# Performance work log

Hardware: AMD Instinct MI355X
Metric: run time of the kernel (lower is better)

Reference implementation:

```python
import jax, jax.numpy as jnp
import numpy as np

N = 50000        # nodes
E = 400000       # edges per relation graph
IN_DIM = 64
HID = 128
OUT_DIM = 2
NSEL = 4096
EPS = 0.3        # residual scale
SLOPE = 0.3      # LeakyReLU negative slope


def _leaky(x):
    return jnp.where(x >= 0, x, SLOPE * x)


def _deg_norm(dst):
    # FAGCN-style d = in_degree^{-1/2}; 0 for isolated nodes
    deg = jax.ops.segment_sum(jnp.ones(dst.shape[0], jnp.float32), dst, num_segments=N)
    return jnp.where(deg > 0, jax.lax.rsqrt(jnp.maximum(deg, 1.0)), 0.0)


def _gnn_layer(hf, src, dst, d, gw, gb):
    # gate(concat[h_dst, h_src]) computed as per-node projections then edge gather
    D = hf.shape[1]
    s_dst = hf @ gw[:D]   # [N]
    s_src = hf @ gw[D:]   # [N]
    a = jnp.tanh(s_dst[dst] + s_src[src] + gb)        # [E]
    e = a * d[dst] * d[src]                            # [E]
    msg = hf[src] * e[:, None]                         # [E, D]
    return jax.ops.segment_sum(msg, dst, num_segments=N)


def setup_inputs() -> dict:
    key = jax.random.key(0)
    ks = iter(jax.random.split(key, 48))
    def nrm(shape, scale=0.05):
        return jax.random.normal(next(ks), shape, jnp.float32) * scale
    inp = {}
    inp["h"] = jax.random.normal(next(ks), (N, IN_DIM), jnp.float32)
    for i in (1, 2, 3):
        inp[f"src{i}"] = jax.random.randint(next(ks), (E,), 0, N)
        inp[f"dst{i}"] = jax.random.randint(next(ks), (E,), 0, N)
    inp["nodes"] = jax.random.randint(next(ks), (NSEL,), 0, N)
    inp["t1_w"] = nrm((HID, IN_DIM)); inp["t1_b"] = jnp.zeros((HID,), jnp.float32)
    for i in (1, 2, 3):
        inp[f"gate1_{i}_w"] = nrm((2 * HID,)); inp[f"gate1_{i}_b"] = jnp.zeros((), jnp.float32)
        inp[f"gate2_{i}_w"] = nrm((6 * HID,)); inp[f"gate2_{i}_b"] = jnp.zeros((), jnp.float32)
        inp[f"hw1_{i}"] = nrm((HID, HID))
        inp[f"hw2_{i}"] = nrm((3 * HID, HID))
    inp["t2_w"] = nrm((64, 7 * HID + IN_DIM)); inp["t2_b"] = jnp.zeros((64,), jnp.float32)
    inp["t3_w"] = nrm((OUT_DIM, 64)); inp["t3_b"] = jnp.zeros((OUT_DIM,), jnp.float32)
    return inp


def reference(h, src1, dst1, src2, dst2, src3, dst3, nodes,
              t1_w, t1_b,
              gate1_1_w, gate1_1_b, gate1_2_w, gate1_2_b, gate1_3_w, gate1_3_b,
              gate2_1_w, gate2_1_b, gate2_2_w, gate2_2_b, gate2_3_w, gate2_3_b,
              hw1_1, hw1_2, hw1_3, hw2_1, hw2_2, hw2_3,
              t2_w, t2_b, t3_w, t3_b):
    d1, d2, d3 = _deg_norm(dst1), _deg_norm(dst2), _deg_norm(dst3)
    raw0 = h
    raw1 = _leaky(h @ t1_w.T + t1_b)   # [N, HID] (dropout=identity in eval)
    h1_1 = _leaky((EPS * raw1 + _gnn_layer(raw1, src1, dst1, d1, gate1_1_w, gate1_1_b)) @ hw1_1)
    h1_2 = _leaky((EPS * raw1 + _gnn_layer(raw1, src2, dst2, d2, gate1_2_w, gate1_2_b)) @ hw1_2)
    h1_3 = _leaky((EPS * raw1 + _gnn_layer(raw1, src3, dst3, d3, gate1_3_w, gate1_3_b)) @ hw1_3)
    raw2 = jnp.concatenate([h1_1, h1_2, h1_3], axis=1)   # [N, 3*HID]
    h2_1 = _leaky((EPS * raw2 + _gnn_layer(raw2, src1, dst1, d1, gate2_1_w, gate2_1_b)) @ hw2_1)
    h2_2 = _leaky((EPS * raw2 + _gnn_layer(raw2, src2, dst2, d2, gate2_2_w, gate2_2_b)) @ hw2_2)
    h2_3 = _leaky((EPS * raw2 + _gnn_layer(raw2, src3, dst3, d3, gate2_3_w, gate2_3_b)) @ hw2_3)
    hf = jnp.concatenate([h2_1, h2_2, h2_3, raw0, raw1, raw2], axis=1)  # [N, 7*HID+IN_DIM]
    nf = hf[nodes]                                       # [NSEL, 7*HID+IN_DIM]
    s = _leaky(nf @ t2_w.T + t2_b)
    return s @ t3_w.T + t3_b                             # [NSEL, OUT_DIM]
```

## Files before the change

### kernel.cpp

```cpp
#include <hip/hip_runtime.h>
#include <hip/hip_bf16.h>

#define NN 50000
#define NE 400000
#define IND 64
#define HID 128
#define H3 384
#define FDIM 960
#define NSEL 4096
#define EPSF 0.3f
#define SLOPEF 0.3f
#define NBK 196
#define BCAP 4096
#define EPB 4096
#define NOEDGE 0xFFFFFFFFu
#define NBF 98

typedef __attribute__((ext_vector_type(8))) short bfrag;
typedef __attribute__((ext_vector_type(4))) float f4;
typedef __attribute__((ext_vector_type(8))) unsigned short us8;

__device__ __forceinline__ float leaky1(float v){ return v>=0.f? v : SLOPEF*v; }
__device__ __forceinline__ float b2f(unsigned short u){
  return __uint_as_float(((unsigned)u)<<16);
}
__device__ __forceinline__ unsigned short f2b(float v){
  __hip_bfloat16 b = __float2bfloat16(v);
  return *(unsigned short*)&b;
}

__global__ __launch_bounds__(256) void k_fill_prep(
    const int* __restrict__ s0,const int* __restrict__ d0,
    const int* __restrict__ s1,const int* __restrict__ d1,
    const int* __restrict__ s2,const int* __restrict__ d2,
    int* __restrict__ bcnt, unsigned int* __restrict__ pairbuf,
    const float* __restrict__ t1w,
    const float* __restrict__ hw1_0, const float* __restrict__ hw1_1, const float* __restrict__ hw1_2,
    const float* __restrict__ hw2_0, const float* __restrict__ hw2_1, const float* __restrict__ hw2_2,
    const float* __restrict__ t2w, const float* __restrict__ h,
    unsigned short* __restrict__ wt1, unsigned short* __restrict__ w1t,
    unsigned short* __restrict__ w2t, unsigned short* __restrict__ wt2,
    unsigned short* __restrict__ hb)
{
  __shared__ __align__(16) unsigned int lbuf[EPB];
  __shared__ int hist[256];
  __shared__ int lbase[256];
  __shared__ int lcur[256];
  __shared__ int gbase[NBK];
  __shared__ int wsum[4];
  const int t = threadIdx.x;

  if (blockIdx.x < 3*NBF){
    const int r = blockIdx.x / NBF;
    const int bx = blockIdx.x - r*NBF;
    const int* S = (r==0)?s0:((r==1)?s1:s2);
    const int* D = (r==0)?d0:((r==1)?d1:d2);
    const int e0 = bx*EPB;
    hist[t] = 0; lcur[t] = 0;
    __syncthreads();
    unsigned int pv[16];
    #pragma unroll
    for (int j=0;j<4;j++){
      int e = e0 + (j*256 + t)*4;
      if (e < NE){
        int4 sv = *(const int4*)&S[e];
        int4 dv = *(const int4*)&D[e];
        pv[j*4+0] = ((unsigned)dv.x<<16)|(unsigned)sv.x;
        pv[j*4+1] = ((unsigned)dv.y<<16)|(unsigned)sv.y;
        pv[j*4+2] = ((unsigned)dv.z<<16)|(unsigned)sv.z;
        pv[j*4+3] = ((unsigned)dv.w<<16)|(unsigned)sv.w;
      } else {
        pv[j*4+0]=NOEDGE; pv[j*4+1]=NOEDGE; pv[j*4+2]=NOEDGE; pv[j*4+3]=NOEDGE;
      }
    }
    #pragma unroll
    for (int i=0;i<16;i++){
      if (pv[i] != NOEDGE) atomicAdd(&hist[pv[i]>>24], 1);
    }
    __syncthreads();
    {
      int hv = hist[t];
      int lane = t & 63, wid = t >> 6;
      int x = hv;
      #pragma unroll
      for (int d=1; d<64; d<<=1){ int y=__shfl_up(x,(unsigned)d); if(lane>=d) x+=y; }
      if (lane==63) wsum[wid]=x;
      __syncthreads();
      int wpre = 0;
      if (wid>0) wpre += wsum[0];
      if (wid>1) wpre += wsum[1];
      if (wid>2) wpre += wsum[2];
      lbase[t] = wpre + x - hv;
      if (t < NBK){
        int hh = hist[t];
        gbase[t] = (hh>0) ? atomicAdd(&bcnt[r*NBK+t], hh) : 0;
      }
    }
    __syncthreads();
    #pragma unroll
    for (int i=0;i<16;i++){
      if (pv[i] != NOEDGE){
        int b = (int)(pv[i] >> 24);
        int pos = lbase[b] + atomicAdd(&lcur[b], 1);
        lbuf[pos] = pv[i];
      }
    }
    __syncthreads();
    int tot = min(NE - e0, EPB);
    for (int idx = t; idx < tot; idx += 256){
      unsigned int v = lbuf[idx];
      int b = (int)(v >> 24);
      pairbuf[((size_t)(r*NBK + b))*BCAP + gbase[b] + (idx - lbase[b])] = v;
    }
  } else {
    int g = (blockIdx.x - 3*NBF)*256 + t;
    if (g < 8192){
      wt1[g] = f2b(t1w[g]);
    } else if (g < 57344){
      int e = g - 8192;
      int r = e / 16384, q = e - r*16384;
      int n = q >> 7, k = q & 127;
      const float* W = (r==0)?hw1_0:((r==1)?hw1_1:hw1_2);
      w1t[e] = f2b(W[k*HID + n]);
    } else if (g < 204800){
      int e = g - 57344;
      int r = e / 49152, q = e - r*49152;
      int n = q / H3, k = q - n*H3;
      const float* W = (r==0)?hw2_0:((r==1)?hw2_1:hw2_2);
      w2t[e] = f2b(W[k*HID + n]);
    } else if (g < 266240){
      int e = g - 204800;
      wt2[e] = f2b(t2w[e]);
    } else if (g < 666240){
      int q = g - 266240;
      const float4 a = ((const float4*)h)[q*2];
      const float4 b = ((const float4*)h)[q*2+1];
      us8 o;
      o[0]=f2b(a.x); o[1]=f2b(a.y); o[2]=f2b(a.z); o[3]=f2b(a.w);
      o[4]=f2b(b.x); o[5]=f2b(b.y); o[6]=f2b(b.z); o[7]=f2b(b.w);
      *(us8*)&hb[q*8] = o;
    }
  }
}

__global__ __launch_bounds__(256) void k_sort_t1(
    const unsigned int* __restrict__ pairbuf, const int* __restrict__ bcnt,
    int* __restrict__ off, float* __restrict__ dnv, unsigned short* __restrict__ csrc,
    const unsigned short* __restrict__ Ab, const unsigned short* __restrict__ W,
    const float* __restrict__ bias, unsigned short* __restrict__ Cb)
{
  __shared__ __align__(16) char smem[27648];
  const int t = threadIdx.x;

  if (blockIdx.x < 2*NBK + NBK){
    unsigned short* lout = (unsigned short*)smem;
    int* hist = (int*)(smem + 8192);
    int* excl = (int*)(smem + 9216);
    int* cur  = (int*)(smem + 10240);
    int* red  = (int*)(smem + 11264);
    int* wsum = (int*)(smem + 12288);
    const int r = blockIdx.x / NBK;
    const int b = blockIdx.x - r*NBK;
    const int nb0 = b << 8;
    red[t] = (t < b) ? bcnt[r*NBK + t] : 0;
    hist[t] = 0; cur[t] = 0;
    __syncthreads();
    #pragma unroll
    for (int sdv=128; sdv>0; sdv>>=1){
      if (t < sdv) red[t] += red[t+sdv];
      __syncthreads();
    }
    const int bbase = red[0];
    const int cnt = bcnt[r*NBK + b];
    const unsigned int* pb = pairbuf + ((size_t)(r*NBK + b))*BCAP;
    unsigned int pv[16];
    #pragma unroll
    for (int j=0;j<16;j++){
      int e = j*256 + t;
      pv[j] = (e < cnt) ? pb[e] : NOEDGE;
      if (pv[j] != NOEDGE) atomicAdd(&hist[(int)(pv[j]>>16) - nb0], 1);
    }
    __syncthreads();
    {
      int hv = hist[t];
      int lane = t & 63, wid = t >> 6;
      int x = hv;
      #pragma unroll
      for (int d=1; d<64; d<<=1){ int y=__shfl_up(x,(unsigned)d); if(lane>=d) x+=y; }
      if (lane==63) wsum[wid]=x;
      __syncthreads();
      int wpre = 0;
      if (wid>0) wpre += wsum[0];
      if (wid>1) wpre += wsum[1];
      if (wid>2) wpre += wsum[2];
      excl[t] = wpre + x - hv;
    }
    __syncthreads();
    int nidx = nb0 + t;
    if (nidx < NN){
      off[r*(NN+1) + nidx] = bbase + excl[t];
      int g = hist[t];
      dnv[r*NN + nidx] = (g>0) ? rsqrtf((float)g) : 0.f;
    }
    if (b == NBK-1 && t == 0) off[r*(NN+1) + NN] = bbase + cnt;
    #pragma unroll
    for (int j=0;j<16;j++){
      if (pv[j] != NOEDGE){
        int pn = (int)(pv[j] >> 16) - nb0;
        int slot = atomicAdd(&cur[pn], 1);
        lout[excl[pn] + slot] = (unsigned short)(pv[j] & 0xffffu);
      }
    }
    __syncthreads();
    unsigned short* op = csrc + (size_t)r*NE + bbase;
    for (int idx = t; idx < cnt; idx += 256) op[idx] = lout[idx];
  } else {
    short (*As)[72] = (short(*)[72])smem;
    short (*Bs)[72] = (short(*)[72])(smem + 9216);
    const int bm = (blockIdx.x - 3*NBK)*64;
    for (int q = t; q < 64*8; q += 256){
      int row = q >> 3, c8 = q & 7;
      int grow = bm + row; grow = (grow < NN) ? grow : (NN-1);
      *(us8*)&As[row][c8*8] = *(const us8*)&Ab[(size_t)grow*IND + c8*8];
    }
    for (int q = t; q < 128*8; q += 256){
      int n = q >> 3, c8 = q & 7;
      *(us8*)&Bs[n][c8*8] = *(const us8*)&W[n*IND + c8*8];
    }
    __syncthreads();
    const int wid = t >> 6, lane = t & 63;
    const int wrow = (wid & 1)*32, wcol = (wid >> 1)*64;
    const int fr = lane & 15, fq = lane >> 4;
    f4 acc[2][4];
    #pragma unroll
    for (int mi=0;mi<2;mi++)
      #pragma unroll
      for (int ni=0;ni<4;ni++) acc[mi][ni] = (f4){0.f,0.f,0.f,0.f};
    #pragma unroll
    for (int ks=0; ks<2; ks++){
      int kb = ks*32 + fq*8;
      bfrag a[2], b[4];
      #pragma unroll
      for (int mi=0;mi<2;mi++) a[mi] = *(const bfrag*)&As[wrow + mi*16 + fr][kb];
      #pragma unroll
      for (int ni=0;ni<4;ni++) b[ni] = *(const bfrag*)&Bs[wcol + ni*16 + fr][kb];
      #pragma unroll
      for (int mi=0;mi<2;mi++)
        #pragma unroll
        for (int ni=0;ni<4;ni++)
          acc[mi][ni] = __builtin_amdgcn_mfma_f32_16x16x32_bf16(a[mi], b[ni], acc[mi][ni], 0, 0, 0);
    }
    #pragma unroll
    for (int mi=0;mi<2;mi++){
      int row0 = bm + wrow + mi*16 + fq*4;
      #pragma unroll
      for (int j=0;j<4;j++){
        int row = row0 + j;
        if (row < NN){
          #pragma unroll
          for (int ni=0;ni<4;ni++){
            int col = wcol + ni*16 + fr;
            Cb[(size_t)row*HID + col] = f2b(leaky1(acc[mi][ni][j] + bias[col]));
          }
        }
      }
    }
  }
}

__global__ __launch_bounds__(256) void k_mfma128(
    const unsigned short* __restrict__ Abf, const unsigned short* __restrict__ Wt,
    unsigned short* __restrict__ Cb, int M)
{
  __shared__ short As[64][136];
  __shared__ short Bs[128][136];
  const int r = blockIdx.y;
  const unsigned short* Ar = Abf + (size_t)r*M*HID;
  const unsigned short* W  = Wt + (size_t)r*HID*HID;
  const int tid = threadIdx.x;
  const int bm = blockIdx.x*64;

  for (int q = tid; q < 64*16; q += 256){
    int row = q >> 4, c8 = q & 15;
    int grow = bm + row; grow = (grow < M) ? grow : (M-1);
    *(us8*)&As[row][c8*8] = *(const us8*)&Ar[(size_t)grow*HID + c8*8];
  }
  for (int q = tid; q < 128*16; q += 256){
    int n = q >> 4, c8 = q & 15;
    *(us8*)&Bs[n][c8*8] = *(const us8*)&W[n*HID + c8*8];
  }
  __syncthreads();

  const int wid = tid >> 6, lane = tid & 63;
  const int wrow = (wid & 1)*32, wcol = (wid >> 1)*64;
  const int fr = lane & 15, fq = lane >> 4;
  f4 acc[2][4];
  #pragma unroll
  for (int mi=0;mi<2;mi++)
    #pragma unroll
    for (int ni=0;ni<4;ni++) acc[mi][ni] = (f4){0.f,0.f,0.f,0.f};

  #pragma unroll
  for (int ks=0; ks<4; ks++){
    int kb = ks*32 + fq*8;
    bfrag a[2], b[4];
    #pragma unroll
    for (int mi=0;mi<2;mi++) a[mi] = *(const bfrag*)&As[wrow + mi*16 + fr][kb];
    #pragma unroll
    for (int ni=0;ni<4;ni++) b[ni] = *(const bfrag*)&Bs[wcol + ni*16 + fr][kb];
    #pragma unroll
    for (int mi=0;mi<2;mi++)
      #pragma unroll
      for (int ni=0;ni<4;ni++)
        acc[mi][ni] = __builtin_amdgcn_mfma_f32_16x16x32_bf16(a[mi], b[ni], acc[mi][ni], 0, 0, 0);
  }

  const int coff = r*HID;
  #pragma unroll
  for (int mi=0;mi<2;mi++){
    int row0 = bm + wrow + mi*16 + fq*4;
    #pragma unroll
    for (int j=0;j<4;j++){
      int row = row0 + j;
      if (row < M){
        #pragma unroll
        for (int ni=0;ni<4;ni++){
          Cb[(size_t)row*H3 + coff + wcol + ni*16 + fr] = f2b(leaky1(acc[mi][ni][j]));
        }
      }
    }
  }
}

__global__ __launch_bounds__(256) void k_hw2_nf(
    const unsigned short* __restrict__ Abf, const unsigned short* __restrict__ Wt,
    const unsigned short* __restrict__ hb, const unsigned short* __restrict__ raw1b,
    const unsigned short* __restrict__ raw2b, const int* __restrict__ nodes,
    unsigned short* __restrict__ nfb)
{
  __shared__ __align__(16) char smem[23040];
  const int t = threadIdx.x;
  if (blockIdx.x < 3*128){
    short (*As)[72] = (short(*)[72])smem;
    short (*Bs)[72] = (short(*)[72])(smem + 4608);
    const int r = blockIdx.x / 128;
    const int bm = (blockIdx.x - r*128)*32;
    const unsigned short* Ar = Abf + (size_t)r*NSEL*H3;
    const unsigned short* W  = Wt + (size_t)r*HID*H3;
    const int wid = t >> 6, lane = t & 63;
    const int fr = lane & 15, fq = lane >> 4;
    f4 acc[2][2];
    #pragma unroll
    for (int mi=0;mi<2;mi++)
      #pragma unroll
      for (int ni=0;ni<2;ni++) acc[mi][ni] = (f4){0.f,0.f,0.f,0.f};
    for (int kc=0; kc<6; kc++){
      for (int q = t; q < 32*8; q += 256){
        int row = q >> 3, c8 = q & 7;
        *(us8*)&As[row][c8*8] = *(const us8*)&Ar[(size_t)(bm+row)*H3 + kc*64 + c8*8];
      }
      for (int q = t; q < 128*8; q += 256){
        int n = q >> 3, c8 = q & 7;
        *(us8*)&Bs[n][c8*8] = *(const us8*)&W[(size_t)n*H3 + kc*64 + c8*8];
      }
      __syncthreads();
      #pragma unroll
      for (int ks=0; ks<2; ks++){
        int kb = ks*32 + fq*8;
        bfrag a[2], b[2];
        #pragma unroll
        for (int mi=0;mi<2;mi++) a[mi] = *(const bfrag*)&As[mi*16 + fr][kb];
        #pragma unroll
        for (int ni=0;ni<2;ni++) b[ni] = *(const bfrag*)&Bs[wid*32 + ni*16 + fr][kb];
        #pragma unroll
        for (int mi=0;mi<2;mi++)
          #pragma unroll
          for (int ni=0;ni<2;ni++)
            acc[mi][ni] = __builtin_amdgcn_mfma_f32_16x16x32_bf16(a[mi], b[ni], acc[mi][ni], 0, 0, 0);
      }
      __syncthreads();
    }
    #pragma unroll
    for (int mi=0;mi<2;mi++){
      int row0 = bm + mi*16 + fq*4;
      #pragma unroll
      for (int j=0;j<4;j++){
        int i = row0 + j;
        #pragma unroll
        for (int ni=0;ni<2;ni++){
          int col = wid*32 + ni*16 + fr;
          nfb[(size_t)i*FDIM + r*HID + col] = f2b(leaky1(acc[mi][ni][j]));
        }
      }
    }
  } else {
    int g = (blockIdx.x - 3*128)*256 + t;
    if (g < NSEL*72){
      int i = g/72, c = g - i*72;
      int n = nodes[i];
      us8 v; int col;
      if (c < 8)       { v = *(const us8*)&hb[(size_t)n*IND + c*8];           col = 384 + c*8; }
      else if (c < 24) { int q=c-8;  v = *(const us8*)&raw1b[(size_t)n*HID + q*8]; col = 448 + q*8; }
      else             { int q=c-24; v = *(const us8*)&raw2b[(size_t)n*H3  + q*8]; col = 576 + q*8; }
      *(us8*)&nfb[(size_t)i*FDIM + col] = v;
    }
  }
}

__global__ __launch_bounds__(256) void k_t2_final(
    const unsigned short* __restrict__ Abf, const unsigned short* __restrict__ W,
    const float* __restrict__ t2b, const float* __restrict__ t3w,
    const float* __restrict__ t3b, float* __restrict__ outp)
{
  __shared__ __align__(16) char smem[13824];
  short (*As)[72] = (short(*)[72])smem;
  short (*Bs)[72] = (short(*)[72])(smem + 4608);
  float (*sb)[64] = (float(*)[64])smem;
  const int t = threadIdx.x;
  const int bm = blockIdx.x*32;
  const int wid = t >> 6, lane = t & 63;
  const int fr = lane & 15, fq = lane >> 4;
  f4 acc[2];
  acc[0] = (f4){0.f,0.f,0.f,0.f};
  acc[1] = (f4){0.f,0.f,0.f,0.f};

  for (int kc=0; kc<15; kc++){
    for (int q = t; q < 32*8; q += 256){
      int row = q >> 3, c8 = q & 7;
      *(us8*)&As[row][c8*8] = *(const us8*)&Abf[(size_t)(bm+row)*FDIM + kc*64 + c8*8];
    }
    for (int q = t; q < 64*8; q += 256){
      int n = q >> 3, c8 = q & 7;
      *(us8*)&Bs[n][c8*8] = *(const us8*)&W[(size_t)n*FDIM + kc*64 + c8*8];
    }
    __syncthreads();
    #pragma unroll
    for (int ks=0; ks<2; ks++){
      int kb = ks*32 + fq*8;
      bfrag a[2], b;
      a[0] = *(const bfrag*)&As[fr][kb];
      a[1] = *(const bfrag*)&As[16 + fr][kb];
      b = *(const bfrag*)&Bs[wid*16 + fr][kb];
      acc[0] = __builtin_amdgcn_mfma_f32_16x16x32_bf16(a[0], b, acc[0], 0, 0, 0);
      acc[1] = __builtin_amdgcn_mfma_f32_16x16x32_bf16(a[1], b, acc[1], 0, 0, 0);
    }
    __syncthreads();
  }

  #pragma unroll
  for (int mi=0;mi<2;mi++){
    int rloc = mi*16 + fq*4;
    #pragma unroll
    for (int j=0;j<4;j++){
      sb[rloc+j][wid*16 + fr] = acc[mi][j];
    }
  }
  __syncthreads();
  for (int rr = wid*8; rr < wid*8+8; rr++){
    float v = leaky1(sb[rr][lane] + t2b[lane]);
    float a0 = v*t3w[lane], a1 = v*t3w[64+lane];
    #pragma unroll
    for (int sft=32;sft>0;sft>>=1){
      a0 += __shfl_down(a0,(unsigned)sft);
      a1 += __shfl_down(a1,(unsigned)sft);
    }
    if (lane==0){
      int w = bm + rr;
      outp[2*w+0] = a0 + t3b[0];
      outp[2*w+1] = a1 + t3b[1];
    }
  }
}

template<int D>
__global__ __launch_bounds__(256) void k_scores_g(const unsigned short* __restrict__ X,
    const float* __restrict__ g0, const float* __restrict__ g1, const float* __restrict__ g2,
    float* __restrict__ sd, float* __restrict__ ss){
  const int tid = threadIdx.x;
  const int p = tid & 15;
  const int n = blockIdx.x*16 + (tid >> 4);
  const unsigned short* x = X + (size_t)n*D;
  float a0=0,a1=0,a2=0,a3=0,a4=0,a5=0;
  #pragma unroll
  for (int it=0; it<D/128; it++){
    int k = it*128 + p*8;
    us8 u = *(const us8*)&x[k];
    #pragma unroll
    for (int e=0;e<8;e++){
      float v = b2f(u[e]);
      a0 = fmaf(v, g0[k+e],   a0);  a1 = fmaf(v, g0[D+k+e], a1);
      a2 = fmaf(v, g1[k+e],   a2);  a3 = fmaf(v, g1[D+k+e], a3);
      a4 = fmaf(v, g2[k+e],   a4);  a5 = fmaf(v, g2[D+k+e], a5);
    }
  }
  #pragma unroll
  for (int s=8;s>0;s>>=1){
    a0 += __shfl_xor(a0,(unsigned)s); a1 += __shfl_xor(a1,(unsigned)s);
    a2 += __shfl_xor(a2,(unsigned)s); a3 += __shfl_xor(a3,(unsigned)s);
    a4 += __shfl_xor(a4,(unsigned)s); a5 += __shfl_xor(a5,(unsigned)s);
  }
  if (p==0){
    sd[0*NN+n]=a0; ss[0*NN+n]=a1;
    sd[1*NN+n]=a2; ss[1*NN+n]=a3;
    sd[2*NN+n]=a4; ss[2*NN+n]=a5;
  }
}

__global__ __launch_bounds__(256) void k_gather_f3z(
    const unsigned short* __restrict__ Xb,
    const int* __restrict__ off, const unsigned short* __restrict__ csrc,
    const float* __restrict__ sd, const float* __restrict__ ss,
    const float* __restrict__ dnv,
    const float* __restrict__ gb0, const float* __restrict__ gb1, const float* __restrict__ gb2,
    unsigned short* __restrict__ outp){
  const int tid = threadIdx.x;
  const int lane = tid & 63;
  const int wg = lane >> 4;
  const int p  = lane & 15;
  const int n = blockIdx.x*16 + (tid >> 4);
  us8 rv = *(const us8*)&Xb[(size_t)n*HID + p*8];
  int p0a[3], p1a[3];
  #pragma unroll
  for (int r=0;r<3;r++){
    p0a[r] = off[r*(NN+1) + n];
    p1a[r] = off[r*(NN+1) + n + 1];
  }
  float resid[8];
  #pragma unroll
  for (int i=0;i<8;i++) resid[i] = EPSF * b2f(rv[i]);

  for (int r=0;r<3;r++){
    const unsigned short* csr = csrc + (size_t)r*NE;
    const float* ssr = ss + r*NN;
    const float* dnr = dnv + r*NN;
    float gbv = ((r==0)?gb0:((r==1)?gb1:gb2))[0];
    float sd_n = sd[r*NN + n], dn_n = dnr[n];
    float acc[8];
    #pragma unroll
    for (int i=0;i<8;i++) acc[i] = resid[i];
    int p0 = p0a[r], p1 = p1a[r];
    for (int pc=p0; pc<p1; pc+=16){
      int m = min(16, p1-pc);
      int s = 0; float c = 0.f;
      if (p < m){
        s = csr[pc+p];
        c = tanhf(sd_n + ssr[s] + gbv) * dn_n * dnr[s];
      }
      int   sj = __shfl(s, wg*16);
      float cj = __shfl(c, wg*16);
      us8 v = *(const us8*)&Xb[(size_t)sj*HID + p*8];
      for (int j=1;j<=m;j++){
        us8 vn; float cn = 0.f;
        if (j < m){
          int sn = __shfl(s, wg*16+j);
          cn = __shfl(c, wg*16+j);
          vn = *(const us8*)&Xb[(size_t)sn*HID + p*8];
        }
        #pragma unroll
        for (int i=0;i<8;i++) acc[i] = fmaf(cj, b2f(v[i]), acc[i]);
        v = vn; cj = cn;
      }
    }
    us8 o;
    #pragma unroll
    for (int i=0;i<8;i++) o[i] = f2b(acc[i]);
    *(us8*)&outp[((size_t)r*NN + n)*HID + p*8] = o;
  }
}

__global__ __launch_bounds__(256) void k_gather_sel3w2(const unsigned short* __restrict__ Xb,
    const int* __restrict__ nodes,
    const int* __restrict__ off, const unsigned short* __restrict__ csrc,
    const float* __restrict__ sd, const float* __restrict__ ss,
    const float* __restrict__ dnv,
    const float* __restrict__ gb0, const float* __restrict__ gb1, const float* __restrict__ gb2,
    unsigned short* __restrict__ outp){
  const int tid = threadIdx.x;
  const int lane = tid & 63;
  const int wg = lane >> 4;
  const int p  = lane & 15;
  const int i = blockIdx.x*16 + (tid >> 4);
  const int r = blockIdx.y;
  const int n = nodes[i];
  const int* offr = off + r*(NN+1);
  const unsigned short* csr = csrc + (size_t)r*NE;
  const float* ssr = ss + r*NN;
  const float* dnr = dnv + r*NN;
  float gbv = ((r==0)?gb0:((r==1)?gb1:gb2))[0];
  float sd_n = sd[r*NN + n], dn_n = dnr[n];
  float acc[3][8];
  #pragma unroll
  for (int cc=0;cc<3;cc++)
    #pragma unroll
    for (int q=0;q<8;q++) acc[cc][q]=0.f;
  int p0 = offr[n], p1 = offr[n+1];
  for (int pc=p0; pc<p1; pc+=16){
    int m = min(16, p1-pc);
    int s = 0; float c = 0.f;
    if (p < m){
      s = csr[pc+p];
      c = tanhf(sd_n + ssr[s] + gbv) * dn_n * dnr[s];
    }
    int   sj = __shfl(s, wg*16);
    float cj = __shfl(c, wg*16);
    const unsigned short* row = &Xb[(size_t)sj*H3];
    us8 v0 = *(const us8*)&row[0*HID + p*8];
    us8 v1 = *(const us8*)&row[1*HID + p*8];
    us8 v2 = *(const us8*)&row[2*HID + p*8];
    for (int j=1;j<=m;j++){
      us8 n0, n1, n2; float cn = 0.f;
      if (j < m){
        int sn = __shfl(s, wg*16+j);
        cn = __shfl(c, wg*16+j);
        const unsigned short* rw = &Xb[(size_t)sn*H3];
        n0 = *(const us8*)&rw[0*HID + p*8];
        n1 = *(const us8*)&rw[1*HID + p*8];
        n2 = *(const us8*)&rw[2*HID + p*8];
      }
      #pragma unroll
      for (int q=0;q<8;q++){
        acc[0][q] = fmaf(cj, b2f(v0[q]), acc[0][q]);
        acc[1][q] = fmaf(cj, b2f(v1[q]), acc[1][q]);
        acc[2][q] = fmaf(cj, b2f(v2[q]), acc[2][q]);
      }
      v0 = n0; v1 = n1; v2 = n2; cj = cn;
    }
  }
  const unsigned short* xrow = &Xb[(size_t)n*H3];
  unsigned short* orow = &outp[((size_t)r*NSEL + i)*H3];
  #pragma unroll
  for (int cc=0;cc<3;cc++){
    us8 v = *(const us8*)&xrow[cc*HID + p*8];
    us8 o;
    #pragma unroll
    for (int q=0;q<8;q++) o[q] = f2b(fmaf(EPSF, b2f(v[q]), acc[cc][q]));
    *(us8*)&orow[cc*HID + p*8] = o;
  }
}

extern "C" void kernel_launch(void* const* d_in, const int* in_sizes, int n_in,
                              void* d_out, int out_size, void* d_ws, size_t ws_size,
                              hipStream_t stream){
  if (n_in < 32) return;
  const float* h = (const float*)d_in[0];
  const int* src[3] = {(const int*)d_in[1], (const int*)d_in[3], (const int*)d_in[5]};
  const int* dst[3] = {(const int*)d_in[2], (const int*)d_in[4], (const int*)d_in[6]};
  const int* nodes = (const int*)d_in[7];
  const float* t1w = (const float*)d_in[8];
  const float* t1b = (const float*)d_in[9];

  bool dictOrder = (in_sizes[12] == 768);
  const float *g1w[3],*g1b[3],*g2w[3],*g2b[3],*hw1[3],*hw2[3];
  for (int r=0;r<3;r++){
    if (dictOrder){
      int base = 10 + r*6;
      g1w[r]=(const float*)d_in[base+0]; g1b[r]=(const float*)d_in[base+1];
      g2w[r]=(const float*)d_in[base+2]; g2b[r]=(const float*)d_in[base+3];
      hw1[r]=(const float*)d_in[base+4]; hw2[r]=(const float*)d_in[base+5];
    } else {
      g1w[r]=(const float*)d_in[10+2*r]; g1b[r]=(const float*)d_in[11+2*r];
      g2w[r]=(const float*)d_in[16+2*r]; g2b[r]=(const float*)d_in[17+2*r];
      hw1[r]=(const float*)d_in[22+r];   hw2[r]=(const float*)d_in[25+r];
    }
  }
  const float* t2w = (const float*)d_in[28];
  const float* t2b = (const float*)d_in[29];
  const float* t3w = (const float*)d_in[30];
  const float* t3b = (const float*)d_in[31];
  float* outp = (float*)d_out;

  char* w = (char*)d_ws;
  auto carve = [&](size_t bytes)->void*{
    void* p = (void*)w;
    w += ((bytes + 255) & ~size_t(255));
    return p;
  };
  int*   bcnt = (int*)  carve((size_t)1024*4);
  int*   off  = (int*)  carve((size_t)3*(NN+1)*4);
  float* dnv  = (float*)carve((size_t)3*NN*4);
  unsigned short* csrc = (unsigned short*)carve((size_t)3*NE*2);
  float* sd1  = (float*)carve((size_t)3*NN*4);
  float* ss1  = (float*)carve((size_t)3*NN*4);
  float* sd2  = (float*)carve((size_t)3*NN*4);
  float* ss2  = (float*)carve((size_t)3*NN*4);
  unsigned short* wt1 = (unsigned short*)carve((size_t)HID*IND*2);
  unsigned short* w1t = (unsigned short*)carve((size_t)3*HID*HID*2);
  unsigned short* w2t = (unsigned short*)carve((size_t)3*HID*H3*2);
  unsigned short* wt2 = (unsigned short*)carve((size_t)64*FDIM*2);
  unsigned short* hb  = (unsigned short*)carve((size_t)NN*IND*2);
  unsigned short* raw1b = (unsigned short*)carve((size_t)NN*HID*2);
  unsigned short* raw2b = (unsigned short*)carve((size_t)NN*H3*2);
  size_t ubytes = (size_t)3*NN*HID*2;
  float* ureg = (float*)carve(ubytes);
  unsigned int* pairbuf = (unsigned int*)ureg;
  unsigned short* pre1b = (unsigned short*)ureg;
  unsigned short* pre2b = (unsigned short*)ureg;
  unsigned short* nfb = (unsigned short*)carve((size_t)NSEL*FDIM*2);

  hipMemsetAsync(bcnt, 0, (size_t)1024*4, stream);
  k_fill_prep<<<3*NBF + 2603, 256, 0, stream>>>(
      src[0],dst[0],src[1],dst[1],src[2],dst[2], bcnt, pairbuf,
      t1w, hw1[0], hw1[1], hw1[2], hw2[0], hw2[1], hw2[2], t2w, h,
      wt1, w1t, w2t, wt2, hb);
  k_sort_t1<<<3*NBK + (NN+63)/64, 256, 0, stream>>>(
      pairbuf, bcnt, off, dnv, csrc, hb, wt1, t1b, raw1b);

  k_scores_g<HID><<<NN/16, 256, 0, stream>>>(raw1b, g1w[0], g1w[1], g1w[2], sd1, ss1);

  k_gather_f3z<<<NN/16, 256, 0, stream>>>(raw1b, off, csrc,
      sd1, ss1, dnv, g1b[0], g1b[1], g1b[2], pre1b);
  k_mfma128<<<dim3((NN+63)/64, 3), 256, 0, stream>>>(pre1b, w1t, raw2b, NN);

  k_scores_g<H3><<<NN/16, 256, 0, stream>>>(raw2b, g2w[0], g2w[1], g2w[2], sd2, ss2);

  k_gather_sel3w2<<<dim3(NSEL/16, 3), 256, 0, stream>>>(raw2b, nodes, off, csrc,
      sd2, ss2, dnv, g2b[0], g2b[1], g2b[2], pre2b);

  k_hw2_nf<<<3*128 + (NSEL*72+255)/256, 256, 0, stream>>>(
      pre2b, w2t, hb, raw1b, raw2b, nodes, nfb);

  k_t2_final<<<NSEL/32, 256, 0, stream>>>(nfb, wt2, t2b, t3w, t3b, outp);
}
```

Before: 186.1 us.

## Fuse gate score projections into GEMM epilogues, remove separate score kernels

```diff
diff --git a/kernel.cpp b/kernel.cpp
--- a/kernel.cpp
+++ b/kernel.cpp
@@ -147,12 +147,14 @@
     const unsigned int* __restrict__ pairbuf, const int* __restrict__ bcnt,
     int* __restrict__ off, float* __restrict__ dnv, unsigned short* __restrict__ csrc,
     const unsigned short* __restrict__ Ab, const unsigned short* __restrict__ W,
-    const float* __restrict__ bias, unsigned short* __restrict__ Cb)
+    const float* __restrict__ bias, unsigned short* __restrict__ Cb,
+    const float* __restrict__ g1w0, const float* __restrict__ g1w1, const float* __restrict__ g1w2,
+    float* __restrict__ sd1, float* __restrict__ ss1)
 {
-  __shared__ __align__(16) char smem[27648];
+  __shared__ __align__(16) char smem[29184];
   const int t = threadIdx.x;
 
-  if (blockIdx.x < 2*NBK + NBK){
+  if (blockIdx.x < 3*NBK){
     unsigned short* lout = (unsigned short*)smem;
     int* hist = (int*)(smem + 8192);
     int* excl = (int*)(smem + 9216);
@@ -217,6 +219,7 @@
   } else {
     short (*As)[72] = (short(*)[72])smem;
     short (*Bs)[72] = (short(*)[72])(smem + 9216);
+    float* sc = (float*)(smem + 27648);
     const int bm = (blockIdx.x - 3*NBK)*64;
     for (int q = t; q < 64*8; q += 256){
       int row = q >> 3, c8 = q & 7;
@@ -227,6 +230,7 @@
       int n = q >> 3, c8 = q & 7;
       *(us8*)&Bs[n][c8*8] = *(const us8*)&W[n*IND + c8*8];
     }
+    for (int q = t; q < 384; q += 256) sc[q] = 0.f;
     __syncthreads();
     const int wid = t >> 6, lane = t & 63;
     const int wrow = (wid & 1)*32, wcol = (wid >> 1)*64;
@@ -252,82 +256,143 @@
     }
     #pragma unroll
     for (int mi=0;mi<2;mi++){
-      int row0 = bm + wrow + mi*16 + fq*4;
       #pragma unroll
       for (int j=0;j<4;j++){
-        int row = row0 + j;
-        if (row < NN){
+        int rowloc = wrow + mi*16 + fq*4 + j;
+        int row = bm + rowloc;
+        bool ok = row < NN;
+        float l6[6] = {0,0,0,0,0,0};
+        #pragma unroll
+        for (int ni=0;ni<4;ni++){
+          int col = wcol + ni*16 + fr;
+          float v = leaky1(acc[mi][ni][j] + bias[col]);
+          if (ok) Cb[(size_t)row*HID + col] = f2b(v);
+          l6[0] = fmaf(v, g1w0[col],     l6[0]);
+          l6[1] = fmaf(v, g1w0[HID+col], l6[1]);
+          l6[2] = fmaf(v, g1w1[col],     l6[2]);
+          l6[3] = fmaf(v, g1w1[HID+col], l6[3]);
+          l6[4] = fmaf(v, g1w2[col],     l6[4]);
+          l6[5] = fmaf(v, g1w2[HID+col], l6[5]);
+        }
+        #pragma unroll
+        for (int k=0;k<6;k++){
+          l6[k] += __shfl_xor(l6[k], 1);
+          l6[k] += __shfl_xor(l6[k], 2);
+          l6[k] += __shfl_xor(l6[k], 4);
+          l6[k] += __shfl_xor(l6[k], 8);
+        }
+        if (fr == 0){
           #pragma unroll
-          for (int ni=0;ni<4;ni++){
-            int col = wcol + ni*16 + fr;
-            Cb[(size_t)row*HID + col] = f2b(leaky1(acc[mi][ni][j] + bias[col]));
-          }
+          for (int k=0;k<6;k++) atomicAdd(&sc[rowloc*6 + k], l6[k]);
         }
       }
     }
-  }
-}
-
-__global__ __launch_bounds__(256) void k_mfma128(
+    __syncthreads();
+    if (t < 64){
+      int row = bm + t;
+      if (row < NN){
+        sd1[0*NN+row] = sc[t*6+0]; ss1[0*NN+row] = sc[t*6+1];
+        sd1[1*NN+row] = sc[t*6+2]; ss1[1*NN+row] = sc[t*6+3];
+        sd1[2*NN+row] = sc[t*6+4]; ss1[2*NN+row] = sc[t*6+5];
+      }
+    }
+  }
+}
+
+__global__ __launch_bounds__(256) void k_mfma128s(
     const unsigned short* __restrict__ Abf, const unsigned short* __restrict__ Wt,
-    unsigned short* __restrict__ Cb, int M)
+    const float* __restrict__ g2w0, const float* __restrict__ g2w1, const float* __restrict__ g2w2,
+    unsigned short* __restrict__ Cb, float* __restrict__ sd2, float* __restrict__ ss2, int M)
 {
   __shared__ short As[64][136];
   __shared__ short Bs[128][136];
-  const int r = blockIdx.y;
-  const unsigned short* Ar = Abf + (size_t)r*M*HID;
-  const unsigned short* W  = Wt + (size_t)r*HID*HID;
+  __shared__ float sc[384];
   const int tid = threadIdx.x;
   const int bm = blockIdx.x*64;
-
-  for (int q = tid; q < 64*16; q += 256){
-    int row = q >> 4, c8 = q & 15;
-    int grow = bm + row; grow = (grow < M) ? grow : (M-1);
-    *(us8*)&As[row][c8*8] = *(const us8*)&Ar[(size_t)grow*HID + c8*8];
-  }
-  for (int q = tid; q < 128*16; q += 256){
-    int n = q >> 4, c8 = q & 15;
-    *(us8*)&Bs[n][c8*8] = *(const us8*)&W[n*HID + c8*8];
-  }
-  __syncthreads();
-
   const int wid = tid >> 6, lane = tid & 63;
   const int wrow = (wid & 1)*32, wcol = (wid >> 1)*64;
   const int fr = lane & 15, fq = lane >> 4;
-  f4 acc[2][4];
-  #pragma unroll
-  for (int mi=0;mi<2;mi++)
-    #pragma unroll
-    for (int ni=0;ni<4;ni++) acc[mi][ni] = (f4){0.f,0.f,0.f,0.f};
-
-  #pragma unroll
-  for (int ks=0; ks<4; ks++){
-    int kb = ks*32 + fq*8;
-    bfrag a[2], b[4];
-    #pragma unroll
-    for (int mi=0;mi<2;mi++) a[mi] = *(const bfrag*)&As[wrow + mi*16 + fr][kb];
-    #pragma unroll
-    for (int ni=0;ni<4;ni++) b[ni] = *(const bfrag*)&Bs[wcol + ni*16 + fr][kb];
+
+  for (int q = tid; q < 384; q += 256) sc[q] = 0.f;
+
+  for (int rc=0; rc<3; rc++){
+    const unsigned short* Ar = Abf + (size_t)rc*M*HID;
+    const unsigned short* W  = Wt + (size_t)rc*HID*HID;
+    for (int q = tid; q < 64*16; q += 256){
+      int row = q >> 4, c8 = q & 15;
+      int grow = bm + row; grow = (grow < M) ? grow : (M-1);
+      *(us8*)&As[row][c8*8] = *(const us8*)&Ar[(size_t)grow*HID + c8*8];
+    }
+    for (int q = tid; q < 128*16; q += 256){
+      int n = q >> 4, c8 = q & 15;
+      *(us8*)&Bs[n][c8*8] = *(const us8*)&W[n*HID + c8*8];
+    }
+    __syncthreads();
+
+    f4 acc[2][4];
     #pragma unroll
     for (int mi=0;mi<2;mi++)
       #pragma unroll
-      for (int ni=0;ni<4;ni++)
-        acc[mi][ni] = __builtin_amdgcn_mfma_f32_16x16x32_bf16(a[mi], b[ni], acc[mi][ni], 0, 0, 0);
-  }
-
-  const int coff = r*HID;
-  #pragma unroll
-  for (int mi=0;mi<2;mi++){
-    int row0 = bm + wrow + mi*16 + fq*4;
-    #pragma unroll
-    for (int j=0;j<4;j++){
-      int row = row0 + j;
-      if (row < M){
+      for (int ni=0;ni<4;ni++) acc[mi][ni] = (f4){0.f,0.f,0.f,0.f};
+    #pragma unroll
+    for (int ks=0; ks<4; ks++){
+      int kb = ks*32 + fq*8;
+      bfrag a[2], b[4];
+      #pragma unroll
+      for (int mi=0;mi<2;mi++) a[mi] = *(const bfrag*)&As[wrow + mi*16 + fr][kb];
+      #pragma unroll
+      for (int ni=0;ni<4;ni++) b[ni] = *(const bfrag*)&Bs[wcol + ni*16 + fr][kb];
+      #pragma unroll
+      for (int mi=0;mi<2;mi++)
+        #pragma unroll
+        for (int ni=0;ni<4;ni++)
+          acc[mi][ni] = __builtin_amdgcn_mfma_f32_16x16x32_bf16(a[mi], b[ni], acc[mi][ni], 0, 0, 0);
+    }
+
+    const int coff = rc*HID;
+    #pragma unroll
+    for (int mi=0;mi<2;mi++){
+      #pragma unroll
+      for (int j=0;j<4;j++){
+        int rowloc = wrow + mi*16 + fq*4 + j;
+        int row = bm + rowloc;
+        bool ok = row < M;
+        float l6[6] = {0,0,0,0,0,0};
         #pragma unroll
         for (int ni=0;ni<4;ni++){
-          Cb[(size_t)row*H3 + coff + wcol + ni*16 + fr] = f2b(leaky1(acc[mi][ni][j]));
+          int col = wcol + ni*16 + fr;
+          float v = leaky1(acc[mi][ni][j]);
+          if (ok) Cb[(size_t)row*H3 + coff + col] = f2b(v);
+          int gc = coff + col;
+          l6[0] = fmaf(v, g2w0[gc],    l6[0]);
+          l6[1] = fmaf(v, g2w0[H3+gc], l6[1]);
+          l6[2] = fmaf(v, g2w1[gc],    l6[2]);
+          l6[3] = fmaf(v, g2w1[H3+gc], l6[3]);
+          l6[4] = fmaf(v, g2w2[gc],    l6[4]);
+          l6[5] = fmaf(v, g2w2[H3+gc], l6[5]);
         }
-      }
+        #pragma unroll
+        for (int k=0;k<6;k++){
+          l6[k] += __shfl_xor(l6[k], 1);
+          l6[k] += __shfl_xor(l6[k], 2);
+          l6[k] += __shfl_xor(l6[k], 4);
+          l6[k] += __shfl_xor(l6[k], 8);
+        }
+        if (fr == 0){
+          #pragma unroll
+          for (int k=0;k<6;k++) atomicAdd(&sc[rowloc*6 + k], l6[k]);
+        }
+      }
+    }
+    __syncthreads();
+  }
+
+  if (tid < 64){
+    int row = bm + tid;
+    if (row < M){
+      sd2[0*NN+row] = sc[tid*6+0]; ss2[0*NN+row] = sc[tid*6+1];
+      sd2[1*NN+row] = sc[tid*6+2]; ss2[1*NN+row] = sc[tid*6+3];
+      sd2[2*NN+row] = sc[tid*6+4]; ss2[2*NN+row] = sc[tid*6+5];
     }
   }
 }
@@ -469,40 +534,6 @@
       outp[2*w+0] = a0 + t3b[0];
       outp[2*w+1] = a1 + t3b[1];
     }
-  }
-}
-
-template<int D>
-__global__ __launch_bounds__(256) void k_scores_g(const unsigned short* __restrict__ X,
-    const float* __restrict__ g0, const float* __restrict__ g1, const float* __restrict__ g2,
-    float* __restrict__ sd, float* __restrict__ ss){
-  const int tid = threadIdx.x;
-  const int p = tid & 15;
-  const int n = blockIdx.x*16 + (tid >> 4);
-  const unsigned short* x = X + (size_t)n*D;
-  float a0=0,a1=0,a2=0,a3=0,a4=0,a5=0;
-  #pragma unroll
-  for (int it=0; it<D/128; it++){
-    int k = it*128 + p*8;
-    us8 u = *(const us8*)&x[k];
-    #pragma unroll
-    for (int e=0;e<8;e++){
-      float v = b2f(u[e]);
-      a0 = fmaf(v, g0[k+e],   a0);  a1 = fmaf(v, g0[D+k+e], a1);
-      a2 = fmaf(v, g1[k+e],   a2);  a3 = fmaf(v, g1[D+k+e], a3);
-      a4 = fmaf(v, g2[k+e],   a4);  a5 = fmaf(v, g2[D+k+e], a5);
-    }
-  }
-  #pragma unroll
-  for (int s=8;s>0;s>>=1){
-    a0 += __shfl_xor(a0,(unsigned)s); a1 += __shfl_xor(a1,(unsigned)s);
-    a2 += __shfl_xor(a2,(unsigned)s); a3 += __shfl_xor(a3,(unsigned)s);
-    a4 += __shfl_xor(a4,(unsigned)s); a5 += __shfl_xor(a5,(unsigned)s);
-  }
-  if (p==0){
-    sd[0*NN+n]=a0; ss[0*NN+n]=a1;
-    sd[1*NN+n]=a2; ss[1*NN+n]=a3;
-    sd[2*NN+n]=a4; ss[2*NN+n]=a5;
   }
 }
 
@@ -703,15 +734,14 @@
       t1w, hw1[0], hw1[1], hw1[2], hw2[0], hw2[1], hw2[2], t2w, h,
       wt1, w1t, w2t, wt2, hb);
   k_sort_t1<<<3*NBK + (NN+63)/64, 256, 0, stream>>>(
-      pairbuf, bcnt, off, dnv, csrc, hb, wt1, t1b, raw1b);
-
-  k_scores_g<HID><<<NN/16, 256, 0, stream>>>(raw1b, g1w[0], g1w[1], g1w[2], sd1, ss1);
+      pairbuf, bcnt, off, dnv, csrc, hb, wt1, t1b, raw1b,
+      g1w[0], g1w[1], g1w[2], sd1, ss1);
 
   k_gather_f3z<<<NN/16, 256, 0, stream>>>(raw1b, off, csrc,
       sd1, ss1, dnv, g1b[0], g1b[1], g1b[2], pre1b);
-  k_mfma128<<<dim3((NN+63)/64, 3), 256, 0, stream>>>(pre1b, w1t, raw2b, NN);
-
-  k_scores_g<H3><<<NN/16, 256, 0, stream>>>(raw2b, g2w[0], g2w[1], g2w[2], sd2, ss2);
+
+  k_mfma128s<<<(NN+63)/64, 256, 0, stream>>>(pre1b, w1t,
+      g2w[0], g2w[1], g2w[2], raw2b, sd2, ss2, NN);
 
   k_gather_sel3w2<<<dim3(NSEL/16, 3), 256, 0, stream>>>(raw2b, nodes, off, csrc,
       sd2, ss2, dnv, g2b[0], g2b[1], g2b[2], pre2b);
```

After: 205.6 us. +10.5%, slower.
